# Performance work log

Measured on AMD Instinct MI355X. Metric: run time of the kernel, lower is better.

## Reference

```python
import jax, jax.numpy as jnp
from jax import lax
import numpy as np

B, T, D_IN, H, L, D_OUT = 1024, 512, 6, 128, 3, 1


def _lstm_layer(xs, w_ih, w_hh, b_ih, b_hh):
    """xs: [B, T, Din]; w_ih: [4H, Din]; w_hh: [4H, H]. PyTorch gate order i,f,g,o."""
    Bq = xs.shape[0]
    Hq = w_hh.shape[1]
    # Precompute the input projection for all timesteps (compute-dense part).
    x_proj = jnp.einsum('btd,gd->btg', xs, w_ih) + (b_ih + b_hh)  # [B, T, 4H]

    def step(carry, xp):
        h, c = carry
        gates = xp + h @ w_hh.T  # [B, 4H]
        i, f, g, o = jnp.split(gates, 4, axis=-1)
        i = jax.nn.sigmoid(i)
        f = jax.nn.sigmoid(f)
        g = jnp.tanh(g)
        o = jax.nn.sigmoid(o)
        c = f * c + i * g
        h = o * jnp.tanh(c)
        return (h, c), h

    h0 = jnp.zeros((Bq, Hq), xs.dtype)
    c0 = jnp.zeros((Bq, Hq), xs.dtype)
    (_, _), hs = lax.scan(step, (h0, c0), jnp.swapaxes(x_proj, 0, 1))  # hs: [T, B, H]
    return jnp.swapaxes(hs, 0, 1)  # [B, T, H]


def setup_inputs() -> dict:
    key = jax.random.key(0)
    ks = jax.random.split(key, 16)
    s = 1.0 / np.sqrt(H)  # PyTorch LSTM init scale
    inp = {"x": jax.random.normal(ks[0], (B, T, D_IN), dtype=jnp.float32)}
    din = D_IN
    for l in range(L):
        inp[f"w_ih{l}"] = jax.random.uniform(ks[1 + 4 * l], (4 * H, din), minval=-s, maxval=s, dtype=jnp.float32)
        inp[f"w_hh{l}"] = jax.random.uniform(ks[2 + 4 * l], (4 * H, H), minval=-s, maxval=s, dtype=jnp.float32)
        inp[f"b_ih{l}"] = jax.random.uniform(ks[3 + 4 * l], (4 * H,), minval=-s, maxval=s, dtype=jnp.float32)
        inp[f"b_hh{l}"] = jax.random.uniform(ks[4 + 4 * l], (4 * H,), minval=-s, maxval=s, dtype=jnp.float32)
        din = H
    inp["fc_w"] = jax.random.uniform(ks[13], (D_OUT, H), minval=-s, maxval=s, dtype=jnp.float32)
    inp["fc_b"] = jax.random.uniform(ks[14], (D_OUT,), minval=-s, maxval=s, dtype=jnp.float32)
    return inp


def reference(x, w_ih0, w_hh0, b_ih0, b_hh0, w_ih1, w_hh1, b_ih1, b_hh1,
              w_ih2, w_hh2, b_ih2, b_hh2, fc_w, fc_b):
    # 3-layer LSTM (inference: dropout between layers is identity) + final Linear on last timestep.
    h = _lstm_layer(x, w_ih0, w_hh0, b_ih0, b_hh0)
    h = _lstm_layer(h, w_ih1, w_hh1, b_ih1, b_hh1)
    h = _lstm_layer(h, w_ih2, w_hh2, b_ih2, b_hh2)
    return h[:, -1, :] @ fc_w.T + fc_b  # [B, 1]
```

## Files before the change

kernel.cpp:

```cpp
#include <hip/hip_runtime.h>

#define TLEN  512
#define HID   128
#define RSLOT 16

typedef __attribute__((ext_vector_type(8))) short          bf16x8;
typedef __attribute__((ext_vector_type(4))) float          f32x4;
typedef __attribute__((ext_vector_type(4))) unsigned short u16x4;
typedef unsigned long long u64;

#define LOG2E  1.4426950408889634f
#define LOG2E2 2.8853900817779268f

__device__ __forceinline__ unsigned short f2bf(float f) {
    union { float f; unsigned u; } v; v.f = f;
    unsigned r = v.u + 0x7fffu + ((v.u >> 16) & 1u);
    return (unsigned short)(r >> 16);
}
__device__ __forceinline__ unsigned short f2bf_fast(float f) {
    union { float f; unsigned u; } v; v.f = f;
    return (unsigned short)((v.u + 0x8000u) >> 16);
}

__device__ __forceinline__ float sig_ps(float xs) {
    return __builtin_amdgcn_rcpf(1.0f + __builtin_exp2f(-xs));
}
__device__ __forceinline__ float tanh_ps(float xs) {
    return 2.0f * __builtin_amdgcn_rcpf(1.0f + __builtin_exp2f(-xs)) - 1.0f;
}

__device__ __forceinline__ int flag_peek(const int* f) {
    return __hip_atomic_load(f, __ATOMIC_RELAXED, __HIP_MEMORY_SCOPE_AGENT);
}
__device__ __forceinline__ int flag_spin(const int* f, int v) {
    int x = flag_peek(f);
    while (x < v) { __builtin_amdgcn_s_sleep(1); x = flag_peek(f); }
    return x;
}
__device__ __forceinline__ void flag_pub(int* f, int v) {
    __hip_atomic_store(f, v, __ATOMIC_RELAXED, __HIP_MEMORY_SCOPE_WORKGROUP);
}

template<int MODE, bool CONS, bool PROD, bool WFC>
__device__ __forceinline__ void run_layer_p(
    const float* __restrict__ xin,
    const u64* __restrict__ rin, u64* __restrict__ rout,
    const int* pin_flag, int* cout_flag, const int* cin_flag, int* pout_flag,
    const float* __restrict__ wih, const float* __restrict__ whh,
    const float* __restrict__ bih, const float* __restrict__ bhh,
    unsigned short (* __restrict__ hbuf)[2048],
    unsigned short (* __restrict__ xbuf)[2048],
    float* __restrict__ fcred,
    const int tid, const int wave, const int lane,
    const int n16, const int quad, const int bbase)
{
    constexpr int NKTX = MODE ? 4 : 1;
    constexpr int DINL = MODE ? 128 : 6;

    bf16x8 Wfx[4][NKTX], Wfh[4][4];
    float  bb[4];
#pragma unroll
    for (int g = 0; g < 4; ++g) {
        const float sc = (g == 2) ? LOG2E2 : LOG2E;
        const int row = g * 128 + wave * 16 + n16;
        bb[g] = (bih[row] + bhh[row]) * sc;
#pragma unroll
        for (int kt = 0; kt < NKTX; ++kt) {
            bf16x8 wv;
#pragma unroll
            for (int j = 0; j < 8; ++j) {
                const int k = kt * 32 + quad * 8 + j;
                wv[j] = (short)f2bf(((k < DINL) ? wih[row * DINL + k] : 0.0f) * sc);
            }
            Wfx[g][kt] = wv;
        }
#pragma unroll
        for (int kt = 0; kt < 4; ++kt) {
            bf16x8 wv;
#pragma unroll
            for (int j = 0; j < 8; ++j) {
                const int k = kt * 32 + quad * 8 + j;
                wv[j] = (short)f2bf(whh[row * HID + k] * sc);
            }
            Wfh[g][kt] = wv;
        }
    }

    { u16x4 z = {0, 0, 0, 0}; *(u16x4*)&hbuf[0][tid * 4] = z; }
    u64 q0 = 0, q1 = 0, q2 = 0, qn = 0;
    float pfx0 = 0.0f;
    int pend = 0, cpend = 0;
    const int xm = tid >> 5, xk = tid & 31;
    if constexpr (CONS) {
        flag_spin(pin_flag, 1);
        *(u64*)&xbuf[0][tid * 4] =
            __hip_atomic_load(rin + tid, __ATOMIC_RELAXED, __HIP_MEMORY_SCOPE_AGENT);
        flag_spin(pin_flag, 2);
        *(u64*)&xbuf[1][tid * 4] =
            __hip_atomic_load(rin + 512 + tid, __ATOMIC_RELAXED, __HIP_MEMORY_SCOPE_AGENT);
        pend = flag_spin(pin_flag, 5);
        q0 = __hip_atomic_load(rin + 2 * 512 + tid, __ATOMIC_RELAXED, __HIP_MEMORY_SCOPE_AGENT);
        q1 = __hip_atomic_load(rin + 3 * 512 + tid, __ATOMIC_RELAXED, __HIP_MEMORY_SCOPE_AGENT);
        q2 = __hip_atomic_load(rin + 4 * 512 + tid, __ATOMIC_RELAXED, __HIP_MEMORY_SCOPE_AGENT);
    } else {
        const int ei = ((xk >> 3) * 16 + xm) * 8 + (xk & 7);
        float v0 = (xk < DINL) ? xin[((bbase + xm) * TLEN + 0) * DINL + xk] : 0.0f;
        float v1 = (xk < DINL) ? xin[((bbase + xm) * TLEN + 1) * DINL + xk] : 0.0f;
        xbuf[0][ei] = f2bf(v0);
        xbuf[1][ei] = f2bf(v1);
        if (xk < DINL) pfx0 = xin[((bbase + xm) * TLEN + 2) * DINL + xk];
    }
    if constexpr (PROD) cpend = -(1 << 30);
    __syncthreads();

    f32x4 accA[4], accB[4];
#pragma unroll
    for (int g = 0; g < 4; ++g) { f32x4 bi = {bb[g], bb[g], bb[g], bb[g]}; accA[g] = bi; }
#pragma unroll
    for (int kt = 0; kt < NKTX; ++kt) {
        bf16x8 a = *(const bf16x8*)&xbuf[0][kt * 512 + lane * 8];
#pragma unroll
        for (int g = 0; g < 4; ++g)
            accA[g] = __builtin_amdgcn_mfma_f32_16x16x32_bf16(a, Wfx[g][kt], accA[g], 0, 0, 0);
    }

    float cst[4] = {0.f, 0.f, 0.f, 0.f};
    int rd = 1, wr = 2;

    auto step = [&](f32x4 (&accC)[4], f32x4 (&accN)[4], int t) {
        const int cur = t & 1, nxt = cur ^ 1;
        __syncthreads();

        if constexpr (CONS) {
            if (t + 5 < TLEN) {
                if (pend < t + 6) pend = flag_spin(pin_flag, t + 6);
                qn = __hip_atomic_load(rin + ((t + 5) & (RSLOT - 1)) * 512 + tid,
                                       __ATOMIC_RELAXED, __HIP_MEMORY_SCOPE_AGENT);
                pend = flag_peek(pin_flag);
            }
        }
        if (tid == 0) {
            if constexpr (CONS) if ((t & 3) == 0) flag_pub(cout_flag, t + 5);
            if constexpr (PROD) if (t >= 2)       flag_pub(pout_flag, t - 1);
        }
        if constexpr (PROD) {
            if (t >= 1) {
                const int e = t - 1;
                if ((e & 3) == 0 && e + 4 > RSLOT && cpend < e + 4 - RSLOT)
                    cpend = flag_spin(cin_flag, e + 4 - RSLOT);
                u64 hv = *(const u64*)&hbuf[cur][tid * 4];
                __hip_atomic_store(rout + (e & (RSLOT - 1)) * 512 + tid, hv,
                                   __ATOMIC_RELAXED, __HIP_MEMORY_SCOPE_WORKGROUP);
                if ((e & 3) == 1) cpend = flag_peek(cin_flag);
            }
        }
        float pfx1 = 0.0f;
        if constexpr (!CONS) {
            if (t + 3 < TLEN && xk < DINL)
                pfx1 = xin[((bbase + xm) * TLEN + (t + 3)) * DINL + xk];
        }

#pragma unroll
        for (int kt = 0; kt < 4; ++kt) {
            bf16x8 a = *(const bf16x8*)&hbuf[cur][kt * 512 + lane * 8];
#pragma unroll
            for (int g = 0; g < 4; ++g)
                accC[g] = __builtin_amdgcn_mfma_f32_16x16x32_bf16(a, Wfh[g][kt], accC[g], 0, 0, 0);
        }

        if (t + 1 < TLEN) {
#pragma unroll
            for (int g = 0; g < 4; ++g) { f32x4 bi = {bb[g], bb[g], bb[g], bb[g]}; accN[g] = bi; }
#pragma unroll
            for (int kt = 0; kt < NKTX; ++kt) {
                bf16x8 a = *(const bf16x8*)&xbuf[rd][kt * 512 + lane * 8];
#pragma unroll
                for (int g = 0; g < 4; ++g)
                    accN[g] = __builtin_amdgcn_mfma_f32_16x16x32_bf16(a, Wfx[g][kt], accN[g], 0, 0, 0);
            }
        }

        unsigned short hb[4]; float hf[4];
#pragma unroll
        for (int r = 0; r < 4; ++r) {
            const float iv = sig_ps (accC[0][r]);
            const float fv = sig_ps (accC[1][r]);
            const float gv = tanh_ps(accC[2][r]);
            const float ov = sig_ps (accC[3][r]);
            const float c  = fv * cst[r] + iv * gv;
            cst[r] = c;
            const float h  = ov * tanh_ps(c * LOG2E2);
            hf[r] = h;
            hb[r] = f2bf_fast(h);
        }
        {
            const int j  = wave * 16 + n16;
            const int eb = (j >> 5) * 512 + (((j & 31) >> 3) * 16) * 8 + ((j & 31) & 7);
#pragma unroll
            for (int r = 0; r < 4; ++r)
                hbuf[nxt][eb + (quad * 4 + r) * 8] = hb[r];
        }
        if constexpr (WFC) {
            if (t == TLEN - 1)
#pragma unroll
                for (int r = 0; r < 4; ++r)
                    fcred[(quad * 4 + r) * HID + wave * 16 + n16] = hf[r];
        }
        if (t + 2 < TLEN) {
            if constexpr (CONS) {
                *(u64*)&xbuf[wr][tid * 4] = q0;
                q0 = q1; q1 = q2; q2 = qn;
            } else {
                xbuf[wr][((xk >> 3) * 16 + xm) * 8 + (xk & 7)] = f2bf(pfx0);
                pfx0 = pfx1;
            }
        }
        rd = wr; wr = (wr == 2) ? 0 : wr + 1;
    };

    for (int t = 0; t < TLEN; t += 2) {
        step(accA, accB, t);
        step(accB, accA, t + 1);
    }

    if constexpr (PROD) {
        __syncthreads();
        if (tid == 0) flag_pub(pout_flag, TLEN - 1);
        {
            flag_spin(cin_flag, TLEN - RSLOT);
            u64 hv = *(const u64*)&hbuf[TLEN & 1][tid * 4];
            __hip_atomic_store(rout + ((TLEN - 1) & (RSLOT - 1)) * 512 + tid, hv,
                               __ATOMIC_RELAXED, __HIP_MEMORY_SCOPE_WORKGROUP);
        }
        __syncthreads();
        if (tid == 0) flag_pub(pout_flag, TLEN);
    }
}

extern "C" __global__ __launch_bounds__(512, 1)
void lstm3_pipe_kernel(const float* __restrict__ xin,
    const float* __restrict__ wih0, const float* __restrict__ whh0,
    const float* __restrict__ bih0, const float* __restrict__ bhh0,
    const float* __restrict__ wih1, const float* __restrict__ whh1,
    const float* __restrict__ bih1, const float* __restrict__ bhh1,
    const float* __restrict__ wih2, const float* __restrict__ whh2,
    const float* __restrict__ bih2, const float* __restrict__ bhh2,
    const float* __restrict__ fcw, const float* __restrict__ fcb,
    float* __restrict__ out,
    int* __restrict__ flags, u64* __restrict__ ring0, u64* __restrict__ ring1)
{
    __shared__ unsigned short hbuf[2][2048];
    __shared__ unsigned short xbuf[3][2048];
    __shared__ float fcred[16 * HID];

    const int tid   = threadIdx.x;
    const int wave  = tid >> 6;
    const int lane  = tid & 63;
    const int n16   = lane & 15;
    const int quad  = lane >> 4;

    const int xcd    = blockIdx.x & 7;
    const int grp    = blockIdx.x >> 3;
    const int layer  = grp % 3;
    const int sgroup = grp / 3;
    const int slice  = sgroup * 8 + xcd;
    const int bbase  = slice * 16;

    u64* r0 = ring0 + (size_t)slice * (RSLOT * 512);
    u64* r1 = ring1 + (size_t)slice * (RSLOT * 512);
    int* prod0 = flags + (size_t)(0 * 64 + slice) * 64;
    int* prod1 = flags + (size_t)(1 * 64 + slice) * 64;
    int* cons1 = flags + (size_t)(2 * 64 + slice) * 64;
    int* cons2 = flags + (size_t)(3 * 64 + slice) * 64;

    if (layer == 0) {
        run_layer_p<0, false, true, false>(xin, nullptr, r0,
            nullptr, nullptr, cons1, prod0,
            wih0, whh0, bih0, bhh0, hbuf, xbuf, fcred, tid, wave, lane, n16, quad, bbase);
    } else if (layer == 1) {
        run_layer_p<1, true, true, false>(nullptr, r0, r1,
            prod0, cons1, cons2, prod1,
            wih1, whh1, bih1, bhh1, hbuf, xbuf, fcred, tid, wave, lane, n16, quad, bbase);
    } else {
        run_layer_p<1, true, false, true>(nullptr, r1, nullptr,
            prod1, cons2, nullptr, nullptr,
            wih2, whh2, bih2, bhh2, hbuf, xbuf, fcred, tid, wave, lane, n16, quad, bbase);
        __syncthreads();
        if (tid < 16) {
            float s = 0.0f;
#pragma unroll 8
            for (int j = 0; j < HID; ++j) s += fcw[j] * fcred[tid * HID + j];
            out[bbase + tid] = s + fcb[0];
        }
    }
}

extern "C" void kernel_launch(void* const* d_in, const int* in_sizes, int n_in,
                              void* d_out, int out_size, void* d_ws, size_t ws_size,
                              hipStream_t stream) {
    (void)in_sizes; (void)n_in; (void)out_size; (void)ws_size;
    const float* x    = (const float*)d_in[0];
    const float* wih0 = (const float*)d_in[1];
    const float* whh0 = (const float*)d_in[2];
    const float* bih0 = (const float*)d_in[3];
    const float* bhh0 = (const float*)d_in[4];
    const float* wih1 = (const float*)d_in[5];
    const float* whh1 = (const float*)d_in[6];
    const float* bih1 = (const float*)d_in[7];
    const float* bhh1 = (const float*)d_in[8];
    const float* wih2 = (const float*)d_in[9];
    const float* whh2 = (const float*)d_in[10];
    const float* bih2 = (const float*)d_in[11];
    const float* bhh2 = (const float*)d_in[12];
    const float* fcw  = (const float*)d_in[13];
    const float* fcb  = (const float*)d_in[14];
    float* out = (float*)d_out;

    int* flags = (int*)d_ws;
    u64* ring0 = (u64*)((char*)d_ws + 65536);
    u64* ring1 = ring0 + (size_t)64 * RSLOT * 512;

    lstm3_pipe_kernel<<<dim3(192), dim3(512), 0, stream>>>(
        x, wih0, whh0, bih0, bhh0, wih1, whh1, bih1, bhh1,
        wih2, whh2, bih2, bhh2, fcw, fcb, out, flags, ring0, ring1);
}
```

Measured before the change: 843.5 us.

## Swizzle LDS buffers, hoist h loads, interleave input-projection MFMAs with gate math

XOR-swizzles the LDS layout of the h and x staging buffers (reads, writes and ring copies) to cut bank conflicts. All h operand loads are hoisted to the start of each step. The next step's input-projection MFMAs are interleaved into the per-row gate activation loop so matrix work overlaps transcendental math. The last two timesteps are peeled through compile-time flags to drop runtime bounds checks. This adds index arithmetic and relies on swizzle consistency between producer and consumer blocks, which both use the same uof mapping.

```diff
diff --git a/kernel.cpp b/kernel.cpp
--- a/kernel.cpp
+++ b/kernel.cpp
@@ -12,6 +12,8 @@
 #define LOG2E  1.4426950408889634f
 #define LOG2E2 2.8853900817779268f
 
+template<bool B> struct BC { static constexpr bool value = B; };
+
 __device__ __forceinline__ unsigned short f2bf(float f) {
     union { float f; unsigned u; } v; v.f = f;
     unsigned r = v.u + 0x7fffu + ((v.u >> 16) & 1u);
@@ -28,6 +30,7 @@
 __device__ __forceinline__ float tanh_ps(float xs) {
     return 2.0f * __builtin_amdgcn_rcpf(1.0f + __builtin_exp2f(-xs)) - 1.0f;
 }
+
 
 __device__ __forceinline__ int flag_peek(const int* f) {
     return __hip_atomic_load(f, __ATOMIC_RELAXED, __HIP_MEMORY_SCOPE_AGENT);
@@ -86,28 +89,37 @@
         }
     }
 
-    { u16x4 z = {0, 0, 0, 0}; *(u16x4*)&hbuf[0][tid * 4] = z; }
+    const int rof  = (lane ^ quad) * 8;
+    const int j    = wave * 16 + n16;
+    const int beta = ((j & 31) >> 3) & 3;
+    const int wbase = ((j >> 5) * 64 + ((j & 31) >> 3) * 16 + quad * 4) * 8 + (j & 7);
+    int wof[4];
+#pragma unroll
+    for (int r = 0; r < 4; ++r) wof[r] = wbase + ((r ^ beta) * 8);
+    const int uof  = ((((tid >> 1) ^ ((tid >> 5) & 3))) << 3) + (tid & 1) * 4;
+    const int xm = tid >> 5, xk = tid & 31;
+    const int eiS = ((xk >> 3) * 16 + (xm ^ (xk >> 3))) * 8 + (xk & 7);
+
+    { u16x4 z = {0, 0, 0, 0}; *(u16x4*)&hbuf[0][uof] = z; }
     u64 q0 = 0, q1 = 0, q2 = 0, qn = 0;
     float pfx0 = 0.0f;
     int pend = 0, cpend = 0;
-    const int xm = tid >> 5, xk = tid & 31;
     if constexpr (CONS) {
         flag_spin(pin_flag, 1);
-        *(u64*)&xbuf[0][tid * 4] =
+        *(u64*)&xbuf[0][uof] =
             __hip_atomic_load(rin + tid, __ATOMIC_RELAXED, __HIP_MEMORY_SCOPE_AGENT);
         flag_spin(pin_flag, 2);
-        *(u64*)&xbuf[1][tid * 4] =
+        *(u64*)&xbuf[1][uof] =
             __hip_atomic_load(rin + 512 + tid, __ATOMIC_RELAXED, __HIP_MEMORY_SCOPE_AGENT);
         pend = flag_spin(pin_flag, 5);
         q0 = __hip_atomic_load(rin + 2 * 512 + tid, __ATOMIC_RELAXED, __HIP_MEMORY_SCOPE_AGENT);
         q1 = __hip_atomic_load(rin + 3 * 512 + tid, __ATOMIC_RELAXED, __HIP_MEMORY_SCOPE_AGENT);
         q2 = __hip_atomic_load(rin + 4 * 512 + tid, __ATOMIC_RELAXED, __HIP_MEMORY_SCOPE_AGENT);
     } else {
-        const int ei = ((xk >> 3) * 16 + xm) * 8 + (xk & 7);
         float v0 = (xk < DINL) ? xin[((bbase + xm) * TLEN + 0) * DINL + xk] : 0.0f;
         float v1 = (xk < DINL) ? xin[((bbase + xm) * TLEN + 1) * DINL + xk] : 0.0f;
-        xbuf[0][ei] = f2bf(v0);
-        xbuf[1][ei] = f2bf(v1);
+        xbuf[0][eiS] = f2bf(v0);
+        xbuf[1][eiS] = f2bf(v1);
         if (xk < DINL) pfx0 = xin[((bbase + xm) * TLEN + 2) * DINL + xk];
     }
     if constexpr (PROD) cpend = -(1 << 30);
@@ -118,18 +130,28 @@
     for (int g = 0; g < 4; ++g) { f32x4 bi = {bb[g], bb[g], bb[g], bb[g]}; accA[g] = bi; }
 #pragma unroll
     for (int kt = 0; kt < NKTX; ++kt) {
-        bf16x8 a = *(const bf16x8*)&xbuf[0][kt * 512 + lane * 8];
+        bf16x8 a = *(const bf16x8*)&xbuf[0][rof + kt * 512];
 #pragma unroll
         for (int g = 0; g < 4; ++g)
             accA[g] = __builtin_amdgcn_mfma_f32_16x16x32_bf16(a, Wfx[g][kt], accA[g], 0, 0, 0);
     }
 
     float cst[4] = {0.f, 0.f, 0.f, 0.f};
+    float hf[4];
     int rd = 1, wr = 2;
 
-    auto step = [&](f32x4 (&accC)[4], f32x4 (&accN)[4], int t) {
+    auto step = [&](auto SHc, auto CMc, f32x4 (&accC)[4], f32x4 (&accN)[4], int t) {
+        constexpr bool SH = decltype(SHc)::value;
+        constexpr bool CM = decltype(CMc)::value;
         const int cur = t & 1, nxt = cur ^ 1;
         __syncthreads();
+
+        const unsigned short* __restrict__ hcur = hbuf[cur];
+        const unsigned short* __restrict__ xrd  = xbuf[rd];
+
+        bf16x8 ha_[4];
+#pragma unroll
+        for (int kt = 0; kt < 4; ++kt) ha_[kt] = *(const bf16x8*)&hcur[rof + kt * 512];
 
         if constexpr (CONS) {
             if (t + 5 < TLEN) {
@@ -148,7 +170,7 @@
                 const int e = t - 1;
                 if ((e & 3) == 0 && e + 4 > RSLOT && cpend < e + 4 - RSLOT)
                     cpend = flag_spin(cin_flag, e + 4 - RSLOT);
-                u64 hv = *(const u64*)&hbuf[cur][tid * 4];
+                u64 hv = *(const u64*)&hcur[uof];
                 __hip_atomic_store(rout + (e & (RSLOT - 1)) * 512 + tid, hv,
                                    __ATOMIC_RELAXED, __HIP_MEMORY_SCOPE_WORKGROUP);
                 if ((e & 3) == 1) cpend = flag_peek(cin_flag);
@@ -161,28 +183,23 @@
         }
 
 #pragma unroll
-        for (int kt = 0; kt < 4; ++kt) {
-            bf16x8 a = *(const bf16x8*)&hbuf[cur][kt * 512 + lane * 8];
+        for (int kt = 0; kt < 4; ++kt)
 #pragma unroll
             for (int g = 0; g < 4; ++g)
-                accC[g] = __builtin_amdgcn_mfma_f32_16x16x32_bf16(a, Wfh[g][kt], accC[g], 0, 0, 0);
-        }
-
-        if (t + 1 < TLEN) {
+                accC[g] = __builtin_amdgcn_mfma_f32_16x16x32_bf16(ha_[kt], Wfh[g][kt], accC[g], 0, 0, 0);
+
+        bf16x8 xa_[2];
+        if constexpr (SH) {
 #pragma unroll
             for (int g = 0; g < 4; ++g) { f32x4 bi = {bb[g], bb[g], bb[g], bb[g]}; accN[g] = bi; }
-#pragma unroll
-            for (int kt = 0; kt < NKTX; ++kt) {
-                bf16x8 a = *(const bf16x8*)&xbuf[rd][kt * 512 + lane * 8];
-#pragma unroll
-                for (int g = 0; g < 4; ++g)
-                    accN[g] = __builtin_amdgcn_mfma_f32_16x16x32_bf16(a, Wfx[g][kt], accN[g], 0, 0, 0);
-            }
-        }
-
-        unsigned short hb[4]; float hf[4];
+            xa_[0] = *(const bf16x8*)&xrd[rof];
+        }
 #pragma unroll
         for (int r = 0; r < 4; ++r) {
+            if constexpr (SH) {
+                if (r + 1 < NKTX)
+                    xa_[(r + 1) & 1] = *(const bf16x8*)&xrd[rof + (r + 1) * 512];
+            }
             const float iv = sig_ps (accC[0][r]);
             const float fv = sig_ps (accC[1][r]);
             const float gv = tanh_ps(accC[2][r]);
@@ -190,15 +207,15 @@
             const float c  = fv * cst[r] + iv * gv;
             cst[r] = c;
             const float h  = ov * tanh_ps(c * LOG2E2);
-            hf[r] = h;
-            hb[r] = f2bf_fast(h);
-        }
-        {
-            const int j  = wave * 16 + n16;
-            const int eb = (j >> 5) * 512 + (((j & 31) >> 3) * 16) * 8 + ((j & 31) & 7);
-#pragma unroll
-            for (int r = 0; r < 4; ++r)
-                hbuf[nxt][eb + (quad * 4 + r) * 8] = hb[r];
+            if constexpr (WFC) hf[r] = h;
+            hbuf[nxt][wof[r]] = f2bf_fast(h);
+            if constexpr (SH) {
+                if (r < NKTX) {
+#pragma unroll
+                    for (int g = 0; g < 4; ++g)
+                        accN[g] = __builtin_amdgcn_mfma_f32_16x16x32_bf16(xa_[r & 1], Wfx[g][r], accN[g], 0, 0, 0);
+                }
+            }
         }
         if constexpr (WFC) {
             if (t == TLEN - 1)
@@ -206,29 +223,31 @@
                 for (int r = 0; r < 4; ++r)
                     fcred[(quad * 4 + r) * HID + wave * 16 + n16] = hf[r];
         }
-        if (t + 2 < TLEN) {
+        if constexpr (CM) {
             if constexpr (CONS) {
-                *(u64*)&xbuf[wr][tid * 4] = q0;
+                *(u64*)&xbuf[wr][uof] = q0;
                 q0 = q1; q1 = q2; q2 = qn;
             } else {
-                xbuf[wr][((xk >> 3) * 16 + xm) * 8 + (xk & 7)] = f2bf(pfx0);
+                xbuf[wr][eiS] = f2bf(pfx0);
                 pfx0 = pfx1;
             }
         }
         rd = wr; wr = (wr == 2) ? 0 : wr + 1;
     };
 
-    for (int t = 0; t < TLEN; t += 2) {
-        step(accA, accB, t);
-        step(accB, accA, t + 1);
-    }
+    for (int t = 0; t < TLEN - 2; t += 2) {
+        step(BC<true>{}, BC<true>{}, accA, accB, t);
+        step(BC<true>{}, BC<true>{}, accB, accA, t + 1);
+    }
+    step(BC<true>{},  BC<false>{}, accA, accB, TLEN - 2);
+    step(BC<false>{}, BC<false>{}, accB, accA, TLEN - 1);
 
     if constexpr (PROD) {
         __syncthreads();
         if (tid == 0) flag_pub(pout_flag, TLEN - 1);
         {
             flag_spin(cin_flag, TLEN - RSLOT);
-            u64 hv = *(const u64*)&hbuf[TLEN & 1][tid * 4];
+            u64 hv = *(const u64*)&hbuf[TLEN & 1][uof];
             __hip_atomic_store(rout + ((TLEN - 1) & (RSLOT - 1)) * 512 + tid, hv,
                                __ATOMIC_RELAXED, __HIP_MEMORY_SCOPE_WORKGROUP);
         }
```

New measurement: 813.9 us. -3.5%, faster.
